# Kernel optimization log

Hardware: AMD Instinct MI355X
Metric: run time of the kernel (lower is better)

## Reference

```python
import jax, jax.numpy as jnp
import numpy as np

B, N, D, H = 4, 2048, 1024, 16
HD = D // H
LR_SCALE = 0.01  # base step size for the fast-weight test-time update
EPS = 1e-6


def setup_inputs() -> dict:
    key = jax.random.key(0)
    ks = jax.random.split(key, 11)
    s = 0.02
    x = jax.random.normal(ks[0], (B, N, D), jnp.float32)
    Wq = jax.random.normal(ks[1], (D, D), jnp.float32) * s
    Wk = jax.random.normal(ks[2], (D, D), jnp.float32) * s
    Wv = jax.random.normal(ks[3], (D, D), jnp.float32) * s
    Wo = jax.random.normal(ks[4], (D, D), jnp.float32) * s
    w1_init = jax.random.normal(ks[5], (H, HD, HD), jnp.float32) * s  # FastWeightGLU init state
    w3_init = jax.random.normal(ks[6], (H, HD, HD), jnp.float32) * s
    W_lr = jax.random.normal(ks[7], (D, H), jnp.float32) * s  # FastWeightHpGLU lr head
    norm_w = jnp.ones((D,), jnp.float32)  # grouped RMSNorm weight
    Wg1 = jax.random.normal(ks[8], (D, HD), jnp.float32) * s  # output_gate bottleneck
    Wg2 = jax.random.normal(ks[9], (HD, D), jnp.float32) * s
    return dict(x=x, Wq=Wq, Wk=Wk, Wv=Wv, Wo=Wo, w1_init=w1_init,
                w3_init=w3_init, W_lr=W_lr, norm_w=norm_w, Wg1=Wg1, Wg2=Wg2)


def _fast_weight_train(q, k, v, lr, w1_init, w3_init):
    # q,k,v: (b,n,h,hd); lr: (b,n,h); fast weight f(x) = silu(x@W1) * (x@W3)
    b = q.shape[0]
    W1_0 = jnp.broadcast_to(w1_init, (b,) + w1_init.shape)
    W3_0 = jnp.broadcast_to(w3_init, (b,) + w3_init.shape)

    def step(carry, inp):
        W1, W3 = carry
        q_t, k_t, v_t, lr_t = inp  # (b,h,hd), lr_t: (b,h,1)
        h1 = jnp.einsum('bhd,bhde->bhe', k_t, W1)
        h3 = jnp.einsum('bhd,bhde->bhe', k_t, W3)
        sg = jax.nn.sigmoid(h1)
        s1 = h1 * sg  # silu(h1)
        err = s1 * h3 - v_t  # d(0.5||f(k)-v||^2)/df
        dsilu = sg * (1.0 + h1 * (1.0 - sg))
        g1 = err * h3 * dsilu
        g3 = err * s1
        W1 = W1 - lr_t[..., None] * jnp.einsum('bhd,bhe->bhde', k_t, g1)
        W3 = W3 - lr_t[..., None] * jnp.einsum('bhd,bhe->bhde', k_t, g3)
        o1 = jnp.einsum('bhd,bhde->bhe', q_t, W1)
        o3 = jnp.einsum('bhd,bhde->bhe', q_t, W3)
        return (W1, W3), jax.nn.silu(o1) * o3

    xs = (q.transpose(1, 0, 2, 3), k.transpose(1, 0, 2, 3),
          v.transpose(1, 0, 2, 3), lr.transpose(1, 0, 2)[..., None])
    (W1, W3), outs = jax.lax.scan(step, (W1_0, W3_0), xs)
    return outs.transpose(1, 0, 2, 3), (W1, W3)  # (b,n,h,hd)


def reference(x, Wq, Wk, Wv, Wo, w1_init, w3_init, W_lr, norm_w, Wg1, Wg2):
    b, n, d = x.shape
    h = w1_init.shape[0]
    hd = d // h
    q = jax.nn.silu((x @ Wq).reshape(b, n, h, hd))
    k = jax.nn.silu((x @ Wk).reshape(b, n, h, hd))
    v = (x @ Wv).reshape(b, n, h, hd)
    lr = LR_SCALE * jax.nn.sigmoid(x @ W_lr)  # (b,n,h) per-token hyper-param
    out, _ = _fast_weight_train(q, k, v, lr, w1_init, w3_init)
    # grouped RMSNorm (per head) fused with sigmoid output gate
    rms = jax.lax.rsqrt(jnp.mean(out * out, axis=-1, keepdims=True) + EPS)
    out = (out * rms).reshape(b, n, d) * norm_w
    gate = (x @ Wg1) @ Wg2
    out = out * jax.nn.sigmoid(gate)
    return out @ Wo
```

## Files before the change

### kernel.cpp

```cpp
#include <hip/hip_runtime.h>
#include <hip/hip_bf16.h>

#define B_ 4
#define N_ 2048
#define D_ 1024
#define H_ 16
#define HD_ 64
#define MTOT (B_*N_)
#define CH_ 16
#define NCH_ (N_/CH_)

typedef __attribute__((ext_vector_type(8))) short short8v;
typedef __attribute__((ext_vector_type(4))) float f32x4;

__global__ void k_cast_bf16(const float* __restrict__ in, __hip_bfloat16* __restrict__ out, int n4){
  int i = blockIdx.x*256 + threadIdx.x;
  if (i >= n4) return;
  float4 vv = ((const float4*)in)[i];
  __hip_bfloat16 b0 = __float2bfloat16(vv.x), b1 = __float2bfloat16(vv.y),
                 b2 = __float2bfloat16(vv.z), b3 = __float2bfloat16(vv.w);
  ushort4 o;
  o.x = *(const unsigned short*)&b0; o.y = *(const unsigned short*)&b1;
  o.z = *(const unsigned short*)&b2; o.w = *(const unsigned short*)&b3;
  ((ushort4*)out)[i] = o;
}

__global__ void k_transpose_cast(const float* __restrict__ in, __hip_bfloat16* __restrict__ out,
                                 int R, int C){
  __shared__ float tile[64][65];
  int r0 = blockIdx.y*64, c0 = blockIdx.x*64;
  int tid = threadIdx.x;
  #pragma unroll
  for (int i=0;i<16;i++){ int idx = tid + i*256; int rr = idx>>6, cc = idx&63;
    tile[rr][cc] = in[(size_t)(r0+rr)*C + (c0+cc)]; }
  __syncthreads();
  #pragma unroll
  for (int i=0;i<16;i++){ int idx = tid + i*256; int rr = idx>>6, cc = idx&63;
    out[(size_t)(c0+rr)*R + (r0+cc)] = __float2bfloat16(tile[cc][rr]); }
}

__global__ void k_prep_wgl(const float* __restrict__ Wg1, const float* __restrict__ Wlr,
                           __hip_bfloat16* __restrict__ WgL){
  int idx = blockIdx.x*256 + threadIdx.x;
  int r = idx >> 10, d = idx & 1023;
  float v = 0.f;
  if (r < 64) v = Wg1[(size_t)d*64 + r];
  else if (r < 80) v = Wlr[(size_t)d*16 + (r-64)];
  WgL[idx] = __float2bfloat16(v);
}

__global__ void k_post_gl(const float* __restrict__ proj, __hip_bfloat16* __restrict__ t1,
                          float* __restrict__ lrout){
  int m = blockIdx.x*4 + (threadIdx.x>>6);
  int e = threadIdx.x & 63;
  float val = proj[(size_t)m*128 + e];
  t1[(size_t)m*64 + e] = __float2bfloat16(val);
  if (e < 16){
    float s = proj[(size_t)m*128 + 64 + e];
    lrout[(size_t)m*16 + e] = 0.01f/(1.0f+__expf(-s));
  }
}

__device__ __forceinline__ void gl2lds16(const void* g, void* l){
  __builtin_amdgcn_global_load_lds((const __attribute__((address_space(1))) void*)g,
                                   (__attribute__((address_space(3))) void*)l, 16, 0, 0);
}

template<int ACT, int LAYOUT>
__global__ __launch_bounds__(256,2) void k_gemm_bt2(
    const __hip_bfloat16* __restrict__ A, const __hip_bfloat16* __restrict__ BT,
    float* __restrict__ C, int M, int N, int K)
{
  __shared__ short As[128*32];
  __shared__ short Bs[128*32];
  const int n0 = blockIdx.x*128, m0 = blockIdx.y*128;
  const int tid = threadIdx.x, lane = tid & 63, wid = tid >> 6;
  const int wm = wid >> 1, wn = wid & 1;
  const short* Aps = (const short*)A;
  const short* Bps = (const short*)BT;
  f32x4 acc[4][4] = {};
  const int srow = wid*32 + (lane>>2);
  const int scol = (lane&3)*8;
  const size_t aoff0 = (size_t)(m0+srow)*K + scol;
  const size_t boff0 = (size_t)(n0+srow)*K + scol;
  short* lA = As + wid*1024;
  short* lB = Bs + wid*1024;
  const int row = lane & 15, kq = (lane >> 4)*8;
  for (int kk = 0; kk < K; kk += 32) {
    __syncthreads();
    gl2lds16(Aps + aoff0 + kk,                 lA);
    gl2lds16(Aps + aoff0 + (size_t)16*K + kk,  lA + 512);
    gl2lds16(Bps + boff0 + kk,                 lB);
    gl2lds16(Bps + boff0 + (size_t)16*K + kk,  lB + 512);
    __syncthreads();
    short8v af[4], bfr[4];
    #pragma unroll
    for (int i=0;i<4;i++) af[i]  = *(const short8v*)(As + (wm*64 + i*16 + row)*32 + kq);
    #pragma unroll
    for (int j=0;j<4;j++) bfr[j] = *(const short8v*)(Bs + (wn*64 + j*16 + row)*32 + kq);
    #pragma unroll
    for (int i=0;i<4;i++)
      #pragma unroll
      for (int j=0;j<4;j++)
        acc[i][j] = __builtin_amdgcn_mfma_f32_16x16x32_bf16(af[i], bfr[j], acc[i][j], 0, 0, 0);
  }
  #pragma unroll
  for (int i=0;i<4;i++){
    #pragma unroll
    for (int j=0;j<4;j++){
      int col = n0 + wn*64 + j*16 + (lane & 15);
      #pragma unroll
      for (int qq=0; qq<4; ++qq){
        int rowg = m0 + wm*64 + i*16 + (lane>>4)*4 + qq;
        float val = acc[i][j][qq];
        if (ACT==1) val = val/(1.0f+__expf(-val));
        if (LAYOUT==0) {
          C[(size_t)rowg*N + col] = val;
        } else {
          size_t oidx = ((((size_t)(rowg>>11))*16 + (col>>6))*(size_t)N_ + (size_t)(rowg & 2047))*64
                        + (size_t)(col & 63);
          C[oidx] = val;
        }
      }
    }
  }
}

__device__ __forceinline__ unsigned short bfr16(float x){
  __hip_bfloat16 b = __float2bfloat16(x);
  return *(unsigned short*)&b;
}
__device__ __forceinline__ short8v cvt_frag(const float4 a, const float4 c){
  short8v r;
  r[0]=(short)bfr16(a.x); r[1]=(short)bfr16(a.y); r[2]=(short)bfr16(a.z); r[3]=(short)bfr16(a.w);
  r[4]=(short)bfr16(c.x); r[5]=(short)bfr16(c.y); r[6]=(short)bfr16(c.z); r[7]=(short)bfr16(c.w);
  return r;
}

__global__ __launch_bounds__(256,1) void k_scan8(
    const float* __restrict__ q, const float* __restrict__ k, const float* __restrict__ v,
    const float* __restrict__ lr, const float* __restrict__ w1i, const float* __restrict__ w3i,
    float* __restrict__ so)
{
  const int blk = blockIdx.x;
  const int bh  = blk >> 2;
  const int sl  = blk & 3;
  const int b = bh >> 4, h = bh & 15;
  const int e0 = sl*16;
  const int tid = threadIdx.x, lane = tid & 63, wid = tid >> 6;
  const int tA = lane & 15, ks8 = (lane >> 4)*8;

  __shared__ __align__(16) __hip_bfloat16 Wb1[16*64];
  __shared__ __align__(16) __hip_bfloat16 Wb3[16*64];
  __shared__ __align__(16) float KW1e[256], KW3e[256];
  __shared__ __align__(16) float QW1[256], QW3[256];
  __shared__ __align__(16) float GKK[256], GQK[256];
  __shared__ __align__(16) float C13[512];

  const int we = tid & 15;
  const int wd = (tid >> 4) * 4;
  float w1r[4], w3r[4];
  {
    const float* w1p = w1i + (size_t)h*HD_*HD_ + e0 + we;
    const float* w3p = w3i + (size_t)h*HD_*HD_ + e0 + we;
    #pragma unroll
    for (int j=0;j<4;j++){ w1r[j] = w1p[(size_t)(wd+j)*64]; w3r[j] = w3p[(size_t)(wd+j)*64]; }
  }
  const int mir_off = we*128 + ((wd*2) ^ ((we&7)<<4));
  auto write_mirrors = [&](){
    uint2 p1, p3;
    p1.x = (unsigned)bfr16(w1r[0]) | ((unsigned)bfr16(w1r[1])<<16);
    p1.y = (unsigned)bfr16(w1r[2]) | ((unsigned)bfr16(w1r[3])<<16);
    p3.x = (unsigned)bfr16(w3r[0]) | ((unsigned)bfr16(w3r[1])<<16);
    p3.y = (unsigned)bfr16(w3r[2]) | ((unsigned)bfr16(w3r[3])<<16);
    *(uint2*)((char*)Wb1 + mir_off) = p1;
    *(uint2*)((char*)Wb3 + mir_off) = p3;
  };
  write_mirrors();

  const float* kfb = k + (size_t)bh*N_*64;
  const float* qfb = q + (size_t)bh*N_*64;
  const float* vfb = v + (size_t)bh*N_*64;
  const float* lrp = lr + ((size_t)b*N_)*16 + h;
  float* sob = so + (((size_t)b*N_)*16 + h)*64 + e0;

  auto mir_read = [&](const __hip_bfloat16* Wm, int m)->short8v{
    return *(const short8v*)((const char*)Wm + tA*128 + (((m*32+ks8)*2) ^ ((tA&7)<<4)));
  };

  float4 fA0,fA1,fA2,fA3;
  float4 fB0,fB1,fB2,fB3;
  float  vvr[16], lrr[16];

  if (wid >= 1) {
    const float* xr = ((wid==2) ? qfb : kfb) + (size_t)tA*64;
    fA0 = *(const float4*)(xr+ks8);    fA1 = *(const float4*)(xr+ks8+4);
    fA2 = *(const float4*)(xr+32+ks8); fA3 = *(const float4*)(xr+32+ks8+4);
    if (wid==3){
      const float* qr = qfb + (size_t)tA*64;
      fB0 = *(const float4*)(qr+ks8);    fB1 = *(const float4*)(qr+ks8+4);
      fB2 = *(const float4*)(qr+32+ks8); fB3 = *(const float4*)(qr+32+ks8+4);
    }
  } else if (lane < 16) {
    #pragma unroll
    for (int t=0;t<CH_;++t){
      vvr[t] = vfb[(size_t)t*64 + e0 + lane];
      lrr[t] = lrp[(size_t)t*16];
    }
  }
  __syncthreads();

  #pragma unroll 1
  for (int c = 0; c < NCH_; ++c) {
    const int t0 = c*CH_;

    if (wid == 1) {
      short8v af0 = cvt_frag(fA0,fA1), af1 = cvt_frag(fA2,fA3);
      const int slot = (((lane>>4)*4) ^ ((( tA>>1)&3)<<2));
      f32x4 acc = {};
      acc = __builtin_amdgcn_mfma_f32_16x16x32_bf16(af0, mir_read(Wb1,0), acc, 0,0,0);
      acc = __builtin_amdgcn_mfma_f32_16x16x32_bf16(af1, mir_read(Wb1,1), acc, 0,0,0);
      *(f32x4*)&KW1e[tA*16 + slot] = acc;
      f32x4 ac3 = {};
      ac3 = __builtin_amdgcn_mfma_f32_16x16x32_bf16(af0, mir_read(Wb3,0), ac3, 0,0,0);
      ac3 = __builtin_amdgcn_mfma_f32_16x16x32_bf16(af1, mir_read(Wb3,1), ac3, 0,0,0);
      *(f32x4*)&KW3e[tA*16 + slot] = ac3;
    } else if (wid == 2) {
      short8v af0 = cvt_frag(fA0,fA1), af1 = cvt_frag(fA2,fA3);
      f32x4 acc = {};
      acc = __builtin_amdgcn_mfma_f32_16x16x32_bf16(af0, mir_read(Wb1,0), acc, 0,0,0);
      acc = __builtin_amdgcn_mfma_f32_16x16x32_bf16(af1, mir_read(Wb1,1), acc, 0,0,0);
      #pragma unroll
      for (int qq=0;qq<4;++qq) QW1[((lane>>4)*4+qq)*16 + tA] = acc[qq];
      f32x4 ac3 = {};
      ac3 = __builtin_amdgcn_mfma_f32_16x16x32_bf16(af0, mir_read(Wb3,0), ac3, 0,0,0);
      ac3 = __builtin_amdgcn_mfma_f32_16x16x32_bf16(af1, mir_read(Wb3,1), ac3, 0,0,0);
      #pragma unroll
      for (int qq=0;qq<4;++qq) QW3[((lane>>4)*4+qq)*16 + tA] = ac3[qq];
    } else if (wid == 3) {
      short8v af0 = cvt_frag(fA0,fA1), af1 = cvt_frag(fA2,fA3);
      short8v aq0 = cvt_frag(fB0,fB1), aq1 = cvt_frag(fB2,fB3);
      f32x4 acc = {};
      acc = __builtin_amdgcn_mfma_f32_16x16x32_bf16(af0, af0, acc, 0,0,0);
      acc = __builtin_amdgcn_mfma_f32_16x16x32_bf16(af1, af1, acc, 0,0,0);
      #pragma unroll
      for (int qq=0;qq<4;++qq) GKK[((lane>>4)*4+qq)*16 + tA] = acc[qq];
      f32x4 ac2 = {};
      ac2 = __builtin_amdgcn_mfma_f32_16x16x32_bf16(aq0, af0, ac2, 0,0,0);
      ac2 = __builtin_amdgcn_mfma_f32_16x16x32_bf16(aq1, af1, ac2, 0,0,0);
      #pragma unroll
      for (int qq=0;qq<4;++qq) GQK[((lane>>4)*4+qq)*16 + tA] = ac2[qq];
    }
    __syncthreads();

    const int tn0 = ((c+1 < NCH_) ? c+1 : c) * CH_;
    if (wid >= 1) {
      const float* xr = ((wid==2) ? qfb : kfb) + (size_t)(tn0+tA)*64;
      fA0 = *(const float4*)(xr+ks8);    fA1 = *(const float4*)(xr+ks8+4);
      fA2 = *(const float4*)(xr+32+ks8); fA3 = *(const float4*)(xr+32+ks8+4);
      if (wid==3){
        const float* qr = qfb + (size_t)(tn0+tA)*64;
        fB0 = *(const float4*)(qr+ks8);    fB1 = *(const float4*)(qr+ks8+4);
        fB2 = *(const float4*)(qr+32+ks8); fB3 = *(const float4*)(qr+32+ks8+4);
      }
    } else if (lane < 16) {
      float vvn[16], lrn[16];
      #pragma unroll
      for (int t=0;t<CH_;++t){
        vvn[t] = vfb[(size_t)(tn0+t)*64 + e0 + lane];
        lrn[t] = lrp[(size_t)(tn0+t)*16];
      }
      float a1[16], a3[16];
      const int swr = ((lane>>1)&3)<<2;
      #pragma unroll
      for (int i2=0;i2<4;i2++){
        f32x4 x1 = *(const f32x4*)&KW1e[lane*16 + ((i2*4) ^ swr)];
        f32x4 x3 = *(const f32x4*)&KW3e[lane*16 + ((i2*4) ^ swr)];
        a1[i2*4+0]=x1[0]; a1[i2*4+1]=x1[1]; a1[i2*4+2]=x1[2]; a1[i2*4+3]=x1[3];
        a3[i2*4+0]=x3[0]; a3[i2*4+1]=x3[1]; a3[i2*4+2]=x3[2]; a3[i2*4+3]=x3[3];
      }
      f32x4 grow[3][4];
      #pragma unroll
      for (int i2=0;i2<4;i2++){
        grow[0][i2] = *(const f32x4*)&GKK[ 0 + i2*4];
        grow[1][i2] = *(const f32x4*)&GKK[16 + i2*4];
        grow[2][i2] = *(const f32x4*)&GKK[32 + i2*4];
      }
      #pragma unroll
      for (int t = 0; t < CH_; ++t) {
        const float h1 = a1[t], h3 = a3[t];
        const float sg = 1.0f/(1.0f + __expf(-h1));
        const float s1 = h1*sg;
        const float er = fmaf(s1, h3, -vvr[t]);
        const float ds = sg*fmaf(h1, 1.0f - sg, 1.0f);
        const float lt = lrr[t];
        float2 cc; cc.x = lt*(er*h3*ds); cc.y = lt*(er*s1);
        *(float2*)&C13[(t*16+lane)*2] = cc;
        #pragma unroll
        for (int t2 = t+1; t2 < CH_; ++t2) {
          const float g = grow[t%3][t2>>2][t2&3];
          a1[t2] = fmaf(-g, cc.x, a1[t2]);
          a3[t2] = fmaf(-g, cc.y, a3[t2]);
        }
        if (t + 3 < CH_) {
          #pragma unroll
          for (int i2=0;i2<4;i2++) grow[(t+3)%3][i2] = *(const f32x4*)&GKK[(t+3)*16 + i2*4];
        }
      }
      #pragma unroll
      for (int t=0;t<CH_;++t){ vvr[t]=vvn[t]; lrr[t]=lrn[t]; }
    }
    __syncthreads();

    {
      const int ot = tid >> 4, oe = tid & 15;
      float o1 = QW1[ot*16+oe], o3 = QW3[ot*16+oe];
      #pragma unroll
      for (int s = 0; s < CH_; ++s) {
        const float gl2 = GQK[ot*16+s];
        const float2 cc = *(const float2*)&C13[(s*16+oe)*2];
        const float g = (s <= ot) ? gl2 : 0.0f;
        o1 = fmaf(-g, cc.x, o1);
        o3 = fmaf(-g, cc.y, o3);
      }
      sob[(size_t)(t0+ot)*(H_*HD_) + oe] = (o1/(1.0f + __expf(-o1)))*o3;
    }

    #pragma unroll
    for (int s = 0; s < CH_; ++s) {
      const float2 cc = *(const float2*)&C13[(s*16+we)*2];
      const float4 ks = *(const float4*)(kfb + (size_t)(t0+s)*64 + wd);
      w1r[0] = fmaf(-ks.x, cc.x, w1r[0]); w1r[1] = fmaf(-ks.y, cc.x, w1r[1]);
      w1r[2] = fmaf(-ks.z, cc.x, w1r[2]); w1r[3] = fmaf(-ks.w, cc.x, w1r[3]);
      w3r[0] = fmaf(-ks.x, cc.y, w3r[0]); w3r[1] = fmaf(-ks.y, cc.y, w3r[1]);
      w3r[2] = fmaf(-ks.z, cc.y, w3r[2]); w3r[3] = fmaf(-ks.w, cc.y, w3r[3]);
    }
    write_mirrors();
    __syncthreads();
  }
}

__global__ void k_norm_gate(const float* __restrict__ so, const float* __restrict__ gate,
                            const float* __restrict__ nw, __hip_bfloat16* __restrict__ y)
{
  int idx = blockIdx.x*4 + (threadIdx.x>>6);
  int e = threadIdx.x & 63;
  float o = so[(size_t)idx*64 + e];
  float ss = o*o;
  #pragma unroll
  for (int m=32; m>=1; m>>=1) ss += __shfl_xor(ss, m, 64);
  float rms = rsqrtf(ss*(1.0f/64.0f) + 1e-6f);
  int hh = idx & 15;
  size_t bn = (size_t)(idx >> 4);
  int d = hh*64 + e;
  float g = gate[bn*1024 + d];
  float val = o*rms*nw[d] * (1.0f/(1.0f+__expf(-g)));
  y[bn*1024 + d] = __float2bfloat16(val);
}

extern "C" void kernel_launch(void* const* d_in, const int* in_sizes, int n_in,
                              void* d_out, int out_size, void* d_ws, size_t ws_size,
                              hipStream_t stream)
{
  const float* x   = (const float*)d_in[0];
  const float* Wq  = (const float*)d_in[1];
  const float* Wk  = (const float*)d_in[2];
  const float* Wv  = (const float*)d_in[3];
  const float* Wo  = (const float*)d_in[4];
  const float* w1i = (const float*)d_in[5];
  const float* w3i = (const float*)d_in[6];
  const float* Wlr = (const float*)d_in[7];
  const float* nw  = (const float*)d_in[8];
  const float* Wg1 = (const float*)d_in[9];
  const float* Wg2 = (const float*)d_in[10];
  float* out = (float*)d_out;

  char* p = (char*)d_ws;
  auto take = [&](size_t bytes)->void*{ void* r = (void*)p; p += (bytes + 255) & ~(size_t)255; return r; };
  __hip_bfloat16* xb   = (__hip_bfloat16*)take((size_t)MTOT*D_*2);
  __hip_bfloat16* Wqt  = (__hip_bfloat16*)take((size_t)D_*D_*2);
  __hip_bfloat16* Wkt  = (__hip_bfloat16*)take((size_t)D_*D_*2);
  __hip_bfloat16* Wvt  = (__hip_bfloat16*)take((size_t)D_*D_*2);
  __hip_bfloat16* Wot  = (__hip_bfloat16*)take((size_t)D_*D_*2);
  __hip_bfloat16* Wg2t = (__hip_bfloat16*)take((size_t)D_*HD_*2);
  __hip_bfloat16* WgL  = (__hip_bfloat16*)take((size_t)128*D_*2);
  __hip_bfloat16* t1b  = (__hip_bfloat16*)take((size_t)MTOT*HD_*2);
  float* projt = (float*)take((size_t)MTOT*128*4);
  float* qf  = (float*)take((size_t)MTOT*D_*4);
  float* kf  = (float*)take((size_t)MTOT*D_*4);
  float* vf  = (float*)take((size_t)MTOT*D_*4);
  float* lrb = (float*)take((size_t)MTOT*H_*4);
  float* sob = (float*)take((size_t)MTOT*D_*4);
  __hip_bfloat16* yb = (__hip_bfloat16*)take((size_t)MTOT*D_*2);

  k_cast_bf16<<<MTOT*D_/4/256, 256, 0, stream>>>(x, xb, MTOT*D_/4);
  k_transpose_cast<<<dim3(16,16), 256, 0, stream>>>(Wq, Wqt, D_, D_);
  k_transpose_cast<<<dim3(16,16), 256, 0, stream>>>(Wk, Wkt, D_, D_);
  k_transpose_cast<<<dim3(16,16), 256, 0, stream>>>(Wv, Wvt, D_, D_);
  k_transpose_cast<<<dim3(16,16), 256, 0, stream>>>(Wo, Wot, D_, D_);
  k_transpose_cast<<<dim3(16,1),  256, 0, stream>>>(Wg2, Wg2t, HD_, D_);
  k_prep_wgl<<<512, 256, 0, stream>>>(Wg1, Wlr, WgL);
  k_gemm_bt2<0,0><<<dim3(1,64), 256, 0, stream>>>(xb, WgL, projt, MTOT, 128, D_);
  k_post_gl<<<MTOT/4, 256, 0, stream>>>(projt, t1b, lrb);
  k_gemm_bt2<1,1><<<dim3(8,64), 256, 0, stream>>>(xb, Wqt, qf, MTOT, D_, D_);
  k_gemm_bt2<1,1><<<dim3(8,64), 256, 0, stream>>>(xb, Wkt, kf, MTOT, D_, D_);
  k_gemm_bt2<0,1><<<dim3(8,64), 256, 0, stream>>>(xb, Wvt, vf, MTOT, D_, D_);
  k_gemm_bt2<0,0><<<dim3(8,64), 256, 0, stream>>>(t1b, Wg2t, out, MTOT, D_, HD_);
  k_scan8<<<256, 256, 0, stream>>>(qf, kf, vf, lrb, w1i, w3i, sob);
  k_norm_gate<<<MTOT*H_/4, 256, 0, stream>>>(sob, out, nw, yb);
  k_gemm_bt2<0,0><<<dim3(8,64), 256, 0, stream>>>(yb, Wot, out, MTOT, D_, D_);
}
```

Baseline: 607.6 us.

## Pipeline next-chunk projections in scan with double-buffered LDS and rank-16 correction

```diff
diff --git a/kernel.cpp b/kernel.cpp
--- a/kernel.cpp
+++ b/kernel.cpp
@@ -137,7 +137,7 @@
   return r;
 }
 
-__global__ __launch_bounds__(256,1) void k_scan8(
+__global__ __launch_bounds__(256,1) void k_scan10(
     const float* __restrict__ q, const float* __restrict__ k, const float* __restrict__ v,
     const float* __restrict__ lr, const float* __restrict__ w1i, const float* __restrict__ w3i,
     float* __restrict__ so)
@@ -152,9 +152,10 @@
 
   __shared__ __align__(16) __hip_bfloat16 Wb1[16*64];
   __shared__ __align__(16) __hip_bfloat16 Wb3[16*64];
-  __shared__ __align__(16) float KW1e[256], KW3e[256];
-  __shared__ __align__(16) float QW1[256], QW3[256];
-  __shared__ __align__(16) float GKK[256], GQK[256];
+  __shared__ __align__(16) float KW1e[2][256], KW3e[2][256];
+  __shared__ __align__(16) float QW1[2][256],  QW3[2][256];
+  __shared__ __align__(16) float GKK[2][256],  GQK[2][256];
+  __shared__ __align__(16) float G2KK[256], G2QK[256];
   __shared__ __align__(16) float C13[512];
 
   const int we = tid & 15;
@@ -190,6 +191,7 @@
 
   float4 fA0,fA1,fA2,fA3;
   float4 fB0,fB1,fB2,fB3;
+  short8v kp0, kp1;
   float  vvr[16], lrr[16];
 
   if (wid >= 1) {
@@ -210,60 +212,122 @@
   }
   __syncthreads();
 
+  if (wid == 1) {
+    short8v xa0 = cvt_frag(fA0,fA1), xa1 = cvt_frag(fA2,fA3);
+    const int slot = (((lane>>4)*4) ^ (((tA>>1)&3)<<2));
+    f32x4 acc = {};
+    acc = __builtin_amdgcn_mfma_f32_16x16x32_bf16(xa0, mir_read(Wb1,0), acc, 0,0,0);
+    acc = __builtin_amdgcn_mfma_f32_16x16x32_bf16(xa1, mir_read(Wb1,1), acc, 0,0,0);
+    *(f32x4*)&KW1e[0][tA*16 + slot] = acc;
+    f32x4 ac3 = {};
+    ac3 = __builtin_amdgcn_mfma_f32_16x16x32_bf16(xa0, mir_read(Wb3,0), ac3, 0,0,0);
+    ac3 = __builtin_amdgcn_mfma_f32_16x16x32_bf16(xa1, mir_read(Wb3,1), ac3, 0,0,0);
+    *(f32x4*)&KW3e[0][tA*16 + slot] = ac3;
+  } else if (wid == 2) {
+    short8v xa0 = cvt_frag(fA0,fA1), xa1 = cvt_frag(fA2,fA3);
+    f32x4 acc = {};
+    acc = __builtin_amdgcn_mfma_f32_16x16x32_bf16(xa0, mir_read(Wb1,0), acc, 0,0,0);
+    acc = __builtin_amdgcn_mfma_f32_16x16x32_bf16(xa1, mir_read(Wb1,1), acc, 0,0,0);
+    #pragma unroll
+    for (int qq=0;qq<4;++qq) QW1[0][((lane>>4)*4+qq)*16 + tA] = acc[qq];
+    f32x4 ac3 = {};
+    ac3 = __builtin_amdgcn_mfma_f32_16x16x32_bf16(xa0, mir_read(Wb3,0), ac3, 0,0,0);
+    ac3 = __builtin_amdgcn_mfma_f32_16x16x32_bf16(xa1, mir_read(Wb3,1), ac3, 0,0,0);
+    #pragma unroll
+    for (int qq=0;qq<4;++qq) QW3[0][((lane>>4)*4+qq)*16 + tA] = ac3[qq];
+  } else if (wid == 3) {
+    short8v xa0 = cvt_frag(fA0,fA1), xa1 = cvt_frag(fA2,fA3);
+    short8v qa0 = cvt_frag(fB0,fB1), qa1 = cvt_frag(fB2,fB3);
+    f32x4 acc = {};
+    acc = __builtin_amdgcn_mfma_f32_16x16x32_bf16(xa0, xa0, acc, 0,0,0);
+    acc = __builtin_amdgcn_mfma_f32_16x16x32_bf16(xa1, xa1, acc, 0,0,0);
+    #pragma unroll
+    for (int qq=0;qq<4;++qq) GKK[0][((lane>>4)*4+qq)*16 + tA] = acc[qq];
+    f32x4 ac2 = {};
+    ac2 = __builtin_amdgcn_mfma_f32_16x16x32_bf16(qa0, xa0, ac2, 0,0,0);
+    ac2 = __builtin_amdgcn_mfma_f32_16x16x32_bf16(qa1, xa1, ac2, 0,0,0);
+    #pragma unroll
+    for (int qq=0;qq<4;++qq) GQK[0][((lane>>4)*4+qq)*16 + tA] = ac2[qq];
+    kp0 = xa0; kp1 = xa1;
+  }
+  if (wid >= 1) {
+    const float* xr = ((wid==2) ? qfb : kfb) + (size_t)(CH_+tA)*64;
+    fA0 = *(const float4*)(xr+ks8);    fA1 = *(const float4*)(xr+ks8+4);
+    fA2 = *(const float4*)(xr+32+ks8); fA3 = *(const float4*)(xr+32+ks8+4);
+    if (wid==3){
+      const float* qr = qfb + (size_t)(CH_+tA)*64;
+      fB0 = *(const float4*)(qr+ks8);    fB1 = *(const float4*)(qr+ks8+4);
+      fB2 = *(const float4*)(qr+32+ks8); fB3 = *(const float4*)(qr+32+ks8+4);
+    }
+  }
+  __syncthreads();
+
   #pragma unroll 1
   for (int c = 0; c < NCH_; ++c) {
     const int t0 = c*CH_;
-
-    if (wid == 1) {
-      short8v af0 = cvt_frag(fA0,fA1), af1 = cvt_frag(fA2,fA3);
-      const int slot = (((lane>>4)*4) ^ ((( tA>>1)&3)<<2));
-      f32x4 acc = {};
-      acc = __builtin_amdgcn_mfma_f32_16x16x32_bf16(af0, mir_read(Wb1,0), acc, 0,0,0);
-      acc = __builtin_amdgcn_mfma_f32_16x16x32_bf16(af1, mir_read(Wb1,1), acc, 0,0,0);
-      *(f32x4*)&KW1e[tA*16 + slot] = acc;
-      f32x4 ac3 = {};
-      ac3 = __builtin_amdgcn_mfma_f32_16x16x32_bf16(af0, mir_read(Wb3,0), ac3, 0,0,0);
-      ac3 = __builtin_amdgcn_mfma_f32_16x16x32_bf16(af1, mir_read(Wb3,1), ac3, 0,0,0);
-      *(f32x4*)&KW3e[tA*16 + slot] = ac3;
-    } else if (wid == 2) {
-      short8v af0 = cvt_frag(fA0,fA1), af1 = cvt_frag(fA2,fA3);
-      f32x4 acc = {};
-      acc = __builtin_amdgcn_mfma_f32_16x16x32_bf16(af0, mir_read(Wb1,0), acc, 0,0,0);
-      acc = __builtin_amdgcn_mfma_f32_16x16x32_bf16(af1, mir_read(Wb1,1), acc, 0,0,0);
-      #pragma unroll
-      for (int qq=0;qq<4;++qq) QW1[((lane>>4)*4+qq)*16 + tA] = acc[qq];
-      f32x4 ac3 = {};
-      ac3 = __builtin_amdgcn_mfma_f32_16x16x32_bf16(af0, mir_read(Wb3,0), ac3, 0,0,0);
-      ac3 = __builtin_amdgcn_mfma_f32_16x16x32_bf16(af1, mir_read(Wb3,1), ac3, 0,0,0);
-      #pragma unroll
-      for (int qq=0;qq<4;++qq) QW3[((lane>>4)*4+qq)*16 + tA] = ac3[qq];
-    } else if (wid == 3) {
-      short8v af0 = cvt_frag(fA0,fA1), af1 = cvt_frag(fA2,fA3);
-      short8v aq0 = cvt_frag(fB0,fB1), aq1 = cvt_frag(fB2,fB3);
-      f32x4 acc = {};
-      acc = __builtin_amdgcn_mfma_f32_16x16x32_bf16(af0, af0, acc, 0,0,0);
-      acc = __builtin_amdgcn_mfma_f32_16x16x32_bf16(af1, af1, acc, 0,0,0);
-      #pragma unroll
-      for (int qq=0;qq<4;++qq) GKK[((lane>>4)*4+qq)*16 + tA] = acc[qq];
-      f32x4 ac2 = {};
-      ac2 = __builtin_amdgcn_mfma_f32_16x16x32_bf16(aq0, af0, ac2, 0,0,0);
-      ac2 = __builtin_amdgcn_mfma_f32_16x16x32_bf16(aq1, af1, ac2, 0,0,0);
-      #pragma unroll
-      for (int qq=0;qq<4;++qq) GQK[((lane>>4)*4+qq)*16 + tA] = ac2[qq];
-    }
-    __syncthreads();
-
-    const int tn0 = ((c+1 < NCH_) ? c+1 : c) * CH_;
+    const int p  = c & 1;
+    const int pn = p ^ 1;
+
     if (wid >= 1) {
-      const float* xr = ((wid==2) ? qfb : kfb) + (size_t)(tn0+tA)*64;
-      fA0 = *(const float4*)(xr+ks8);    fA1 = *(const float4*)(xr+ks8+4);
-      fA2 = *(const float4*)(xr+32+ks8); fA3 = *(const float4*)(xr+32+ks8+4);
-      if (wid==3){
-        const float* qr = qfb + (size_t)(tn0+tA)*64;
-        fB0 = *(const float4*)(qr+ks8);    fB1 = *(const float4*)(qr+ks8+4);
-        fB2 = *(const float4*)(qr+32+ks8); fB3 = *(const float4*)(qr+32+ks8+4);
+      if (c+1 < NCH_) {
+        short8v xa0 = cvt_frag(fA0,fA1), xa1 = cvt_frag(fA2,fA3);
+        if (wid == 1) {
+          const int slot = (((lane>>4)*4) ^ (((tA>>1)&3)<<2));
+          f32x4 acc = {};
+          acc = __builtin_amdgcn_mfma_f32_16x16x32_bf16(xa0, mir_read(Wb1,0), acc, 0,0,0);
+          acc = __builtin_amdgcn_mfma_f32_16x16x32_bf16(xa1, mir_read(Wb1,1), acc, 0,0,0);
+          *(f32x4*)&KW1e[pn][tA*16 + slot] = acc;
+          f32x4 ac3 = {};
+          ac3 = __builtin_amdgcn_mfma_f32_16x16x32_bf16(xa0, mir_read(Wb3,0), ac3, 0,0,0);
+          ac3 = __builtin_amdgcn_mfma_f32_16x16x32_bf16(xa1, mir_read(Wb3,1), ac3, 0,0,0);
+          *(f32x4*)&KW3e[pn][tA*16 + slot] = ac3;
+        } else if (wid == 2) {
+          f32x4 acc = {};
+          acc = __builtin_amdgcn_mfma_f32_16x16x32_bf16(xa0, mir_read(Wb1,0), acc, 0,0,0);
+          acc = __builtin_amdgcn_mfma_f32_16x16x32_bf16(xa1, mir_read(Wb1,1), acc, 0,0,0);
+          #pragma unroll
+          for (int qq=0;qq<4;++qq) QW1[pn][((lane>>4)*4+qq)*16 + tA] = acc[qq];
+          f32x4 ac3 = {};
+          ac3 = __builtin_amdgcn_mfma_f32_16x16x32_bf16(xa0, mir_read(Wb3,0), ac3, 0,0,0);
+          ac3 = __builtin_amdgcn_mfma_f32_16x16x32_bf16(xa1, mir_read(Wb3,1), ac3, 0,0,0);
+          #pragma unroll
+          for (int qq=0;qq<4;++qq) QW3[pn][((lane>>4)*4+qq)*16 + tA] = ac3[qq];
+        } else {
+          short8v qa0 = cvt_frag(fB0,fB1), qa1 = cvt_frag(fB2,fB3);
+          f32x4 acc = {};
+          acc = __builtin_amdgcn_mfma_f32_16x16x32_bf16(xa0, xa0, acc, 0,0,0);
+          acc = __builtin_amdgcn_mfma_f32_16x16x32_bf16(xa1, xa1, acc, 0,0,0);
+          #pragma unroll
+          for (int qq=0;qq<4;++qq) GKK[pn][((lane>>4)*4+qq)*16 + tA] = acc[qq];
+          f32x4 ac2 = {};
+          ac2 = __builtin_amdgcn_mfma_f32_16x16x32_bf16(qa0, xa0, ac2, 0,0,0);
+          ac2 = __builtin_amdgcn_mfma_f32_16x16x32_bf16(qa1, xa1, ac2, 0,0,0);
+          #pragma unroll
+          for (int qq=0;qq<4;++qq) GQK[pn][((lane>>4)*4+qq)*16 + tA] = ac2[qq];
+          f32x4 a2k = {};
+          a2k = __builtin_amdgcn_mfma_f32_16x16x32_bf16(xa0, kp0, a2k, 0,0,0);
+          a2k = __builtin_amdgcn_mfma_f32_16x16x32_bf16(xa1, kp1, a2k, 0,0,0);
+          #pragma unroll
+          for (int qq=0;qq<4;++qq) G2KK[((lane>>4)*4+qq)*16 + tA] = a2k[qq];
+          f32x4 a2q = {};
+          a2q = __builtin_amdgcn_mfma_f32_16x16x32_bf16(qa0, kp0, a2q, 0,0,0);
+          a2q = __builtin_amdgcn_mfma_f32_16x16x32_bf16(qa1, kp1, a2q, 0,0,0);
+          #pragma unroll
+          for (int qq=0;qq<4;++qq) G2QK[((lane>>4)*4+qq)*16 + tA] = a2q[qq];
+          kp0 = xa0; kp1 = xa1;
+        }
+        const int tn0 = ((c+2 < NCH_) ? c+2 : NCH_-1) * CH_;
+        const float* xr = ((wid==2) ? qfb : kfb) + (size_t)(tn0+tA)*64;
+        fA0 = *(const float4*)(xr+ks8);    fA1 = *(const float4*)(xr+ks8+4);
+        fA2 = *(const float4*)(xr+32+ks8); fA3 = *(const float4*)(xr+32+ks8+4);
+        if (wid==3){
+          const float* qr = qfb + (size_t)(tn0+tA)*64;
+          fB0 = *(const float4*)(qr+ks8);    fB1 = *(const float4*)(qr+ks8+4);
+          fB2 = *(const float4*)(qr+32+ks8); fB3 = *(const float4*)(qr+32+ks8+4);
+        }
       }
     } else if (lane < 16) {
+      const int tn0 = ((c+1 < NCH_) ? c+1 : c) * CH_;
       float vvn[16], lrn[16];
       #pragma unroll
       for (int t=0;t<CH_;++t){
@@ -274,17 +338,17 @@
       const int swr = ((lane>>1)&3)<<2;
       #pragma unroll
       for (int i2=0;i2<4;i2++){
-        f32x4 x1 = *(const f32x4*)&KW1e[lane*16 + ((i2*4) ^ swr)];
-        f32x4 x3 = *(const f32x4*)&KW3e[lane*16 + ((i2*4) ^ swr)];
+        f32x4 x1 = *(const f32x4*)&KW1e[p][lane*16 + ((i2*4) ^ swr)];
+        f32x4 x3 = *(const f32x4*)&KW3e[p][lane*16 + ((i2*4) ^ swr)];
         a1[i2*4+0]=x1[0]; a1[i2*4+1]=x1[1]; a1[i2*4+2]=x1[2]; a1[i2*4+3]=x1[3];
         a3[i2*4+0]=x3[0]; a3[i2*4+1]=x3[1]; a3[i2*4+2]=x3[2]; a3[i2*4+3]=x3[3];
       }
       f32x4 grow[3][4];
       #pragma unroll
       for (int i2=0;i2<4;i2++){
-        grow[0][i2] = *(const f32x4*)&GKK[ 0 + i2*4];
-        grow[1][i2] = *(const f32x4*)&GKK[16 + i2*4];
-        grow[2][i2] = *(const f32x4*)&GKK[32 + i2*4];
+        grow[0][i2] = *(const f32x4*)&GKK[p][ 0 + i2*4];
+        grow[1][i2] = *(const f32x4*)&GKK[p][16 + i2*4];
+        grow[2][i2] = *(const f32x4*)&GKK[p][32 + i2*4];
       }
       #pragma unroll
       for (int t = 0; t < CH_; ++t) {
@@ -304,7 +368,7 @@
         }
         if (t + 3 < CH_) {
           #pragma unroll
-          for (int i2=0;i2<4;i2++) grow[(t+3)%3][i2] = *(const f32x4*)&GKK[(t+3)*16 + i2*4];
+          for (int i2=0;i2<4;i2++) grow[(t+3)%3][i2] = *(const f32x4*)&GKK[p][(t+3)*16 + i2*4];
         }
       }
       #pragma unroll
@@ -314,28 +378,54 @@
 
     {
       const int ot = tid >> 4, oe = tid & 15;
-      float o1 = QW1[ot*16+oe], o3 = QW3[ot*16+oe];
+      const bool doc = (c+1 < NCH_);
+      float gq[16], g2k[16], g2q[16];
+      #pragma unroll
+      for (int i2=0;i2<4;i2++){
+        f32x4 a = *(const f32x4*)&GQK[p][ot*16 + i2*4];
+        gq[i2*4]=a[0]; gq[i2*4+1]=a[1]; gq[i2*4+2]=a[2]; gq[i2*4+3]=a[3];
+      }
+      if (doc){
+        #pragma unroll
+        for (int i2=0;i2<4;i2++){
+          f32x4 a = *(const f32x4*)&G2KK[ot*16 + i2*4];
+          f32x4 bq = *(const f32x4*)&G2QK[ot*16 + i2*4];
+          g2k[i2*4]=a[0]; g2k[i2*4+1]=a[1]; g2k[i2*4+2]=a[2]; g2k[i2*4+3]=a[3];
+          g2q[i2*4]=bq[0]; g2q[i2*4+1]=bq[1]; g2q[i2*4+2]=bq[2]; g2q[i2*4+3]=bq[3];
+        }
+      }
+      float o1 = QW1[p][ot*16+oe], o3 = QW3[p][ot*16+oe];
+      float ao1=0.f, ao3=0.f, ak1=0.f, ak3=0.f, aq1=0.f, aq3=0.f;
       #pragma unroll
       for (int s = 0; s < CH_; ++s) {
-        const float gl2 = GQK[ot*16+s];
         const float2 cc = *(const float2*)&C13[(s*16+oe)*2];
-        const float g = (s <= ot) ? gl2 : 0.0f;
-        o1 = fmaf(-g, cc.x, o1);
-        o3 = fmaf(-g, cc.y, o3);
-      }
+        const float go = (s <= ot) ? gq[s] : 0.0f;
+        ao1 = fmaf(go, cc.x, ao1);  ao3 = fmaf(go, cc.y, ao3);
+        if (doc){
+          ak1 = fmaf(g2k[s], cc.x, ak1);  ak3 = fmaf(g2k[s], cc.y, ak3);
+          aq1 = fmaf(g2q[s], cc.x, aq1);  aq3 = fmaf(g2q[s], cc.y, aq3);
+        }
+      }
+      o1 -= ao1; o3 -= ao3;
       sob[(size_t)(t0+ot)*(H_*HD_) + oe] = (o1/(1.0f + __expf(-o1)))*o3;
+      if (doc){
+        const int ie = oe*16 + ((((ot>>2)<<2) ^ (((oe>>1)&3)<<2))) + (ot&3);
+        KW1e[pn][ie] -= ak1;
+        KW3e[pn][ie] -= ak3;
+        QW1[pn][ot*16+oe] -= aq1;
+        QW3[pn][ot*16+oe] -= aq3;
+      }
+      #pragma unroll
+      for (int s = 0; s < CH_; ++s) {
+        const float2 cc = *(const float2*)&C13[(s*16+we)*2];
+        const float4 ks = *(const float4*)(kfb + (size_t)(t0+s)*64 + wd);
+        w1r[0] = fmaf(-ks.x, cc.x, w1r[0]); w1r[1] = fmaf(-ks.y, cc.x, w1r[1]);
+        w1r[2] = fmaf(-ks.z, cc.x, w1r[2]); w1r[3] = fmaf(-ks.w, cc.x, w1r[3]);
+        w3r[0] = fmaf(-ks.x, cc.y, w3r[0]); w3r[1] = fmaf(-ks.y, cc.y, w3r[1]);
+        w3r[2] = fmaf(-ks.z, cc.y, w3r[2]); w3r[3] = fmaf(-ks.w, cc.y, w3r[3]);
+      }
+      write_mirrors();
     }
-
-    #pragma unroll
-    for (int s = 0; s < CH_; ++s) {
-      const float2 cc = *(const float2*)&C13[(s*16+we)*2];
-      const float4 ks = *(const float4*)(kfb + (size_t)(t0+s)*64 + wd);
-      w1r[0] = fmaf(-ks.x, cc.x, w1r[0]); w1r[1] = fmaf(-ks.y, cc.x, w1r[1]);
-      w1r[2] = fmaf(-ks.z, cc.x, w1r[2]); w1r[3] = fmaf(-ks.w, cc.x, w1r[3]);
-      w3r[0] = fmaf(-ks.x, cc.y, w3r[0]); w3r[1] = fmaf(-ks.y, cc.y, w3r[1]);
-      w3r[2] = fmaf(-ks.z, cc.y, w3r[2]); w3r[3] = fmaf(-ks.w, cc.y, w3r[3]);
-    }
-    write_mirrors();
     __syncthreads();
   }
 }
@@ -406,7 +496,7 @@
   k_gemm_bt2<1,1><<<dim3(8,64), 256, 0, stream>>>(xb, Wkt, kf, MTOT, D_, D_);
   k_gemm_bt2<0,1><<<dim3(8,64), 256, 0, stream>>>(xb, Wvt, vf, MTOT, D_, D_);
   k_gemm_bt2<0,0><<<dim3(8,64), 256, 0, stream>>>(t1b, Wg2t, out, MTOT, D_, HD_);
-  k_scan8<<<256, 256, 0, stream>>>(qf, kf, vf, lrb, w1i, w3i, sob);
+  k_scan10<<<256, 256, 0, stream>>>(qf, kf, vf, lrb, w1i, w3i, sob);
   k_norm_gate<<<MTOT*H_/4, 256, 0, stream>>>(sob, out, nw, yb);
   k_gemm_bt2<0,0><<<dim3(8,64), 256, 0, stream>>>(yb, Wot, out, MTOT, D_, D_);
 }
```

Result: slower. 626.5 us (+3.1%).

## Collapse fast-weight scan block to a single wavefront with register-resident weights

Applied to the files above, without the earlier changes.

```diff
diff --git a/kernel.cpp b/kernel.cpp
--- a/kernel.cpp
+++ b/kernel.cpp
@@ -137,7 +137,7 @@
   return r;
 }
 
-__global__ __launch_bounds__(256,1) void k_scan8(
+__global__ __launch_bounds__(64,1) void k_scan11(
     const float* __restrict__ q, const float* __restrict__ k, const float* __restrict__ v,
     const float* __restrict__ lr, const float* __restrict__ w1i, const float* __restrict__ w3i,
     float* __restrict__ so)
@@ -147,36 +147,15 @@
   const int sl  = blk & 3;
   const int b = bh >> 4, h = bh & 15;
   const int e0 = sl*16;
-  const int tid = threadIdx.x, lane = tid & 63, wid = tid >> 6;
-  const int tA = lane & 15, ks8 = (lane >> 4)*8;
-
-  __shared__ __align__(16) __hip_bfloat16 Wb1[16*64];
-  __shared__ __align__(16) __hip_bfloat16 Wb3[16*64];
+  const int lane = threadIdx.x;
+  const int tA = lane & 15, g = lane >> 4;
+
   __shared__ __align__(16) float KW1e[256], KW3e[256];
   __shared__ __align__(16) float QW1[256], QW3[256];
   __shared__ __align__(16) float GKK[256], GQK[256];
   __shared__ __align__(16) float C13[512];
-
-  const int we = tid & 15;
-  const int wd = (tid >> 4) * 4;
-  float w1r[4], w3r[4];
-  {
-    const float* w1p = w1i + (size_t)h*HD_*HD_ + e0 + we;
-    const float* w3p = w3i + (size_t)h*HD_*HD_ + e0 + we;
-    #pragma unroll
-    for (int j=0;j<4;j++){ w1r[j] = w1p[(size_t)(wd+j)*64]; w3r[j] = w3p[(size_t)(wd+j)*64]; }
-  }
-  const int mir_off = we*128 + ((wd*2) ^ ((we&7)<<4));
-  auto write_mirrors = [&](){
-    uint2 p1, p3;
-    p1.x = (unsigned)bfr16(w1r[0]) | ((unsigned)bfr16(w1r[1])<<16);
-    p1.y = (unsigned)bfr16(w1r[2]) | ((unsigned)bfr16(w1r[3])<<16);
-    p3.x = (unsigned)bfr16(w3r[0]) | ((unsigned)bfr16(w3r[1])<<16);
-    p3.y = (unsigned)bfr16(w3r[2]) | ((unsigned)bfr16(w3r[3])<<16);
-    *(uint2*)((char*)Wb1 + mir_off) = p1;
-    *(uint2*)((char*)Wb3 + mir_off) = p3;
-  };
-  write_mirrors();
+  __shared__ __align__(16) float vS[256];
+  __shared__ float lrS[16];
 
   const float* kfb = k + (size_t)bh*N_*64;
   const float* qfb = q + (size_t)bh*N_*64;
@@ -184,92 +163,94 @@
   const float* lrp = lr + ((size_t)b*N_)*16 + h;
   float* sob = so + (((size_t)b*N_)*16 + h)*64 + e0;
 
-  auto mir_read = [&](const __hip_bfloat16* Wm, int m)->short8v{
-    return *(const short8v*)((const char*)Wm + tA*128 + (((m*32+ks8)*2) ^ ((tA&7)<<4)));
-  };
-
-  float4 fA0,fA1,fA2,fA3;
-  float4 fB0,fB1,fB2,fB3;
-  float  vvr[16], lrr[16];
-
-  if (wid >= 1) {
-    const float* xr = ((wid==2) ? qfb : kfb) + (size_t)tA*64;
-    fA0 = *(const float4*)(xr+ks8);    fA1 = *(const float4*)(xr+ks8+4);
-    fA2 = *(const float4*)(xr+32+ks8); fA3 = *(const float4*)(xr+32+ks8+4);
-    if (wid==3){
-      const float* qr = qfb + (size_t)tA*64;
-      fB0 = *(const float4*)(qr+ks8);    fB1 = *(const float4*)(qr+ks8+4);
-      fB2 = *(const float4*)(qr+32+ks8); fB3 = *(const float4*)(qr+32+ks8+4);
-    }
-  } else if (lane < 16) {
-    #pragma unroll
-    for (int t=0;t<CH_;++t){
-      vvr[t] = vfb[(size_t)t*64 + e0 + lane];
-      lrr[t] = lrp[(size_t)t*16];
-    }
-  }
-  __syncthreads();
+  float w1m[2][8], w3m[2][8];
+  {
+    const float* w1p = w1i + (size_t)h*HD_*HD_ + e0 + tA;
+    const float* w3p = w3i + (size_t)h*HD_*HD_ + e0 + tA;
+    #pragma unroll
+    for (int m=0;m<2;m++)
+      #pragma unroll
+      for (int j=0;j<8;j++){
+        const int d = m*32 + g*8 + j;
+        w1m[m][j] = w1p[(size_t)d*64];
+        w3m[m][j] = w3p[(size_t)d*64];
+      }
+  }
+  short8v wb1[2], wb3[2];
+  #pragma unroll
+  for (int m=0;m<2;m++){
+    short8v r1, r3;
+    #pragma unroll
+    for (int j=0;j<8;j++){ r1[j]=(short)bfr16(w1m[m][j]); r3[j]=(short)bfr16(w3m[m][j]); }
+    wb1[m]=r1; wb3[m]=r3;
+  }
+
+  float4 kP[4], qP[4]; float vP[4]; float lrP = 0.f;
+  {
+    const float* kr = kfb + (size_t)tA*64 + g*8;
+    const float* qr = qfb + (size_t)tA*64 + g*8;
+    #pragma unroll
+    for (int m=0;m<2;m++){
+      kP[m*2]   = *(const float4*)(kr + m*32);
+      kP[m*2+1] = *(const float4*)(kr + m*32 + 4);
+      qP[m*2]   = *(const float4*)(qr + m*32);
+      qP[m*2+1] = *(const float4*)(qr + m*32 + 4);
+    }
+    #pragma unroll
+    for (int i=0;i<4;i++) vP[i] = vfb[(size_t)(g*4+i)*64 + e0 + tA];
+    if (lane < 16) lrP = lrp[(size_t)lane*16];
+  }
 
   #pragma unroll 1
   for (int c = 0; c < NCH_; ++c) {
     const int t0 = c*CH_;
-
-    if (wid == 1) {
-      short8v af0 = cvt_frag(fA0,fA1), af1 = cvt_frag(fA2,fA3);
-      const int slot = (((lane>>4)*4) ^ ((( tA>>1)&3)<<2));
-      f32x4 acc = {};
-      acc = __builtin_amdgcn_mfma_f32_16x16x32_bf16(af0, mir_read(Wb1,0), acc, 0,0,0);
-      acc = __builtin_amdgcn_mfma_f32_16x16x32_bf16(af1, mir_read(Wb1,1), acc, 0,0,0);
-      *(f32x4*)&KW1e[tA*16 + slot] = acc;
-      f32x4 ac3 = {};
-      ac3 = __builtin_amdgcn_mfma_f32_16x16x32_bf16(af0, mir_read(Wb3,0), ac3, 0,0,0);
-      ac3 = __builtin_amdgcn_mfma_f32_16x16x32_bf16(af1, mir_read(Wb3,1), ac3, 0,0,0);
-      *(f32x4*)&KW3e[tA*16 + slot] = ac3;
-    } else if (wid == 2) {
-      short8v af0 = cvt_frag(fA0,fA1), af1 = cvt_frag(fA2,fA3);
-      f32x4 acc = {};
-      acc = __builtin_amdgcn_mfma_f32_16x16x32_bf16(af0, mir_read(Wb1,0), acc, 0,0,0);
-      acc = __builtin_amdgcn_mfma_f32_16x16x32_bf16(af1, mir_read(Wb1,1), acc, 0,0,0);
-      #pragma unroll
-      for (int qq=0;qq<4;++qq) QW1[((lane>>4)*4+qq)*16 + tA] = acc[qq];
-      f32x4 ac3 = {};
-      ac3 = __builtin_amdgcn_mfma_f32_16x16x32_bf16(af0, mir_read(Wb3,0), ac3, 0,0,0);
-      ac3 = __builtin_amdgcn_mfma_f32_16x16x32_bf16(af1, mir_read(Wb3,1), ac3, 0,0,0);
-      #pragma unroll
-      for (int qq=0;qq<4;++qq) QW3[((lane>>4)*4+qq)*16 + tA] = ac3[qq];
-    } else if (wid == 3) {
-      short8v af0 = cvt_frag(fA0,fA1), af1 = cvt_frag(fA2,fA3);
-      short8v aq0 = cvt_frag(fB0,fB1), aq1 = cvt_frag(fB2,fB3);
-      f32x4 acc = {};
-      acc = __builtin_amdgcn_mfma_f32_16x16x32_bf16(af0, af0, acc, 0,0,0);
-      acc = __builtin_amdgcn_mfma_f32_16x16x32_bf16(af1, af1, acc, 0,0,0);
-      #pragma unroll
-      for (int qq=0;qq<4;++qq) GKK[((lane>>4)*4+qq)*16 + tA] = acc[qq];
-      f32x4 ac2 = {};
-      ac2 = __builtin_amdgcn_mfma_f32_16x16x32_bf16(aq0, af0, ac2, 0,0,0);
-      ac2 = __builtin_amdgcn_mfma_f32_16x16x32_bf16(aq1, af1, ac2, 0,0,0);
-      #pragma unroll
-      for (int qq=0;qq<4;++qq) GQK[((lane>>4)*4+qq)*16 + tA] = ac2[qq];
-    }
-    __syncthreads();
-
-    const int tn0 = ((c+1 < NCH_) ? c+1 : c) * CH_;
-    if (wid >= 1) {
-      const float* xr = ((wid==2) ? qfb : kfb) + (size_t)(tn0+tA)*64;
-      fA0 = *(const float4*)(xr+ks8);    fA1 = *(const float4*)(xr+ks8+4);
-      fA2 = *(const float4*)(xr+32+ks8); fA3 = *(const float4*)(xr+32+ks8+4);
-      if (wid==3){
-        const float* qr = qfb + (size_t)(tn0+tA)*64;
-        fB0 = *(const float4*)(qr+ks8);    fB1 = *(const float4*)(qr+ks8+4);
-        fB2 = *(const float4*)(qr+32+ks8); fB3 = *(const float4*)(qr+32+ks8+4);
-      }
-    } else if (lane < 16) {
-      float vvn[16], lrn[16];
-      #pragma unroll
-      for (int t=0;t<CH_;++t){
-        vvn[t] = vfb[(size_t)(tn0+t)*64 + e0 + lane];
-        lrn[t] = lrp[(size_t)(tn0+t)*16];
-      }
+    #pragma unroll
+    for (int i=0;i<4;i++) vS[(g*4+i)*16 + tA] = vP[i];
+    if (lane < 16) lrS[lane] = lrP;
+    short8v ka0 = cvt_frag(kP[0],kP[1]), ka1 = cvt_frag(kP[2],kP[3]);
+    short8v qa0 = cvt_frag(qP[0],qP[1]), qa1 = cvt_frag(qP[2],qP[3]);
+    const int tn0 = ((c+1 < NCH_) ? (c+1) : c)*CH_;
+    {
+      const float* kr = kfb + (size_t)(tn0+tA)*64 + g*8;
+      const float* qr = qfb + (size_t)(tn0+tA)*64 + g*8;
+      #pragma unroll
+      for (int m=0;m<2;m++){
+        kP[m*2]   = *(const float4*)(kr + m*32);
+        kP[m*2+1] = *(const float4*)(kr + m*32 + 4);
+        qP[m*2]   = *(const float4*)(qr + m*32);
+        qP[m*2+1] = *(const float4*)(qr + m*32 + 4);
+      }
+      #pragma unroll
+      for (int i=0;i<4;i++) vP[i] = vfb[(size_t)(tn0+g*4+i)*64 + e0 + tA];
+      if (lane < 16) lrP = lrp[(size_t)(tn0+lane)*16];
+    }
+    f32x4 aKW1={}, aKW3={}, aQW1={}, aQW3={}, aGKK={}, aGQK={};
+    aKW1 = __builtin_amdgcn_mfma_f32_16x16x32_bf16(ka0, wb1[0], aKW1, 0,0,0);
+    aKW1 = __builtin_amdgcn_mfma_f32_16x16x32_bf16(ka1, wb1[1], aKW1, 0,0,0);
+    aKW3 = __builtin_amdgcn_mfma_f32_16x16x32_bf16(ka0, wb3[0], aKW3, 0,0,0);
+    aKW3 = __builtin_amdgcn_mfma_f32_16x16x32_bf16(ka1, wb3[1], aKW3, 0,0,0);
+    aQW1 = __builtin_amdgcn_mfma_f32_16x16x32_bf16(qa0, wb1[0], aQW1, 0,0,0);
+    aQW1 = __builtin_amdgcn_mfma_f32_16x16x32_bf16(qa1, wb1[1], aQW1, 0,0,0);
+    aQW3 = __builtin_amdgcn_mfma_f32_16x16x32_bf16(qa0, wb3[0], aQW3, 0,0,0);
+    aQW3 = __builtin_amdgcn_mfma_f32_16x16x32_bf16(qa1, wb3[1], aQW3, 0,0,0);
+    aGKK = __builtin_amdgcn_mfma_f32_16x16x32_bf16(ka0, ka0, aGKK, 0,0,0);
+    aGKK = __builtin_amdgcn_mfma_f32_16x16x32_bf16(ka1, ka1, aGKK, 0,0,0);
+    aGQK = __builtin_amdgcn_mfma_f32_16x16x32_bf16(qa0, ka0, aGQK, 0,0,0);
+    aGQK = __builtin_amdgcn_mfma_f32_16x16x32_bf16(qa1, ka1, aGQK, 0,0,0);
+    const int slot = (g*4) ^ (((tA>>1)&3)<<2);
+    *(f32x4*)&KW1e[tA*16 + slot] = aKW1;
+    *(f32x4*)&KW3e[tA*16 + slot] = aKW3;
+    #pragma unroll
+    for (int qq=0;qq<4;++qq){
+      QW1[(g*4+qq)*16 + tA] = aQW1[qq];
+      QW3[(g*4+qq)*16 + tA] = aQW3[qq];
+      GKK[(g*4+qq)*16 + tA] = aGKK[qq];
+      GQK[(g*4+qq)*16 + tA] = aGQK[qq];
+    }
+    asm volatile("s_waitcnt lgkmcnt(0)" ::: "memory");
+    __builtin_amdgcn_sched_barrier(0);
+
+    if (lane < 16) {
       float a1[16], a3[16];
       const int swr = ((lane>>1)&3)<<2;
       #pragma unroll
@@ -291,52 +272,78 @@
         const float h1 = a1[t], h3 = a3[t];
         const float sg = 1.0f/(1.0f + __expf(-h1));
         const float s1 = h1*sg;
-        const float er = fmaf(s1, h3, -vvr[t]);
+        const float er = fmaf(s1, h3, -vS[t*16+lane]);
         const float ds = sg*fmaf(h1, 1.0f - sg, 1.0f);
-        const float lt = lrr[t];
+        const float lt = lrS[t];
         float2 cc; cc.x = lt*(er*h3*ds); cc.y = lt*(er*s1);
         *(float2*)&C13[(t*16+lane)*2] = cc;
         #pragma unroll
         for (int t2 = t+1; t2 < CH_; ++t2) {
-          const float g = grow[t%3][t2>>2][t2&3];
-          a1[t2] = fmaf(-g, cc.x, a1[t2]);
-          a3[t2] = fmaf(-g, cc.y, a3[t2]);
+          const float gg = grow[t%3][t2>>2][t2&3];
+          a1[t2] = fmaf(-gg, cc.x, a1[t2]);
+          a3[t2] = fmaf(-gg, cc.y, a3[t2]);
         }
         if (t + 3 < CH_) {
           #pragma unroll
           for (int i2=0;i2<4;i2++) grow[(t+3)%3][i2] = *(const f32x4*)&GKK[(t+3)*16 + i2*4];
         }
       }
-      #pragma unroll
-      for (int t=0;t<CH_;++t){ vvr[t]=vvn[t]; lrr[t]=lrn[t]; }
-    }
-    __syncthreads();
-
-    {
-      const int ot = tid >> 4, oe = tid & 15;
-      float o1 = QW1[ot*16+oe], o3 = QW3[ot*16+oe];
-      #pragma unroll
-      for (int s = 0; s < CH_; ++s) {
-        const float gl2 = GQK[ot*16+s];
-        const float2 cc = *(const float2*)&C13[(s*16+oe)*2];
-        const float g = (s <= ot) ? gl2 : 0.0f;
-        o1 = fmaf(-g, cc.x, o1);
-        o3 = fmaf(-g, cc.y, o3);
-      }
-      sob[(size_t)(t0+ot)*(H_*HD_) + oe] = (o1/(1.0f + __expf(-o1)))*o3;
-    }
-
-    #pragma unroll
-    for (int s = 0; s < CH_; ++s) {
-      const float2 cc = *(const float2*)&C13[(s*16+we)*2];
-      const float4 ks = *(const float4*)(kfb + (size_t)(t0+s)*64 + wd);
-      w1r[0] = fmaf(-ks.x, cc.x, w1r[0]); w1r[1] = fmaf(-ks.y, cc.x, w1r[1]);
-      w1r[2] = fmaf(-ks.z, cc.x, w1r[2]); w1r[3] = fmaf(-ks.w, cc.x, w1r[3]);
-      w3r[0] = fmaf(-ks.x, cc.y, w3r[0]); w3r[1] = fmaf(-ks.y, cc.y, w3r[1]);
-      w3r[2] = fmaf(-ks.z, cc.y, w3r[2]); w3r[3] = fmaf(-ks.w, cc.y, w3r[3]);
-    }
-    write_mirrors();
-    __syncthreads();
+    }
+    asm volatile("s_waitcnt lgkmcnt(0)" ::: "memory");
+    __builtin_amdgcn_sched_barrier(0);
+
+    float c1r[16], c3r[16];
+    #pragma unroll
+    for (int s=0;s<CH_;++s){
+      float2 cc = *(const float2*)&C13[(s*16+tA)*2];
+      c1r[s]=cc.x; c3r[s]=cc.y;
+    }
+    #pragma unroll
+    for (int i=0;i<4;++i){
+      const int ot = g*4 + i;
+      float o1 = QW1[ot*16+tA], o3 = QW3[ot*16+tA];
+      float gq[16];
+      #pragma unroll
+      for (int i2=0;i2<4;i2++){
+        f32x4 a = *(const f32x4*)&GQK[ot*16 + i2*4];
+        gq[i2*4]=a[0]; gq[i2*4+1]=a[1]; gq[i2*4+2]=a[2]; gq[i2*4+3]=a[3];
+      }
+      #pragma unroll
+      for (int s=0;s<CH_;++s){
+        const float gg = (s <= ot) ? gq[s] : 0.0f;
+        o1 = fmaf(-gg, c1r[s], o1);
+        o3 = fmaf(-gg, c3r[s], o3);
+      }
+      sob[(size_t)(t0+ot)*(H_*HD_) + tA] = (o1/(1.0f + __expf(-o1)))*o3;
+    }
+
+    #pragma unroll
+    for (int s=0;s<CH_;++s){
+      const float* kr = kfb + (size_t)(t0+s)*64 + g*8;
+      const float4 k0 = *(const float4*)(kr);
+      const float4 k1 = *(const float4*)(kr+4);
+      const float4 k2 = *(const float4*)(kr+32);
+      const float4 k3 = *(const float4*)(kr+36);
+      const float c1 = c1r[s], c3 = c3r[s];
+      float kk0[8] = {k0.x,k0.y,k0.z,k0.w,k1.x,k1.y,k1.z,k1.w};
+      float kk1[8] = {k2.x,k2.y,k2.z,k2.w,k3.x,k3.y,k3.z,k3.w};
+      #pragma unroll
+      for (int j=0;j<8;j++){
+        w1m[0][j] = fmaf(-kk0[j], c1, w1m[0][j]);
+        w3m[0][j] = fmaf(-kk0[j], c3, w3m[0][j]);
+        w1m[1][j] = fmaf(-kk1[j], c1, w1m[1][j]);
+        w3m[1][j] = fmaf(-kk1[j], c3, w3m[1][j]);
+      }
+    }
+    #pragma unroll
+    for (int m=0;m<2;m++){
+      short8v r1, r3;
+      #pragma unroll
+      for (int j=0;j<8;j++){ r1[j]=(short)bfr16(w1m[m][j]); r3[j]=(short)bfr16(w3m[m][j]); }
+      wb1[m]=r1; wb3[m]=r3;
+    }
+    asm volatile("s_waitcnt lgkmcnt(0)" ::: "memory");
+    __builtin_amdgcn_sched_barrier(0);
   }
 }
 
@@ -406,7 +413,7 @@
   k_gemm_bt2<1,1><<<dim3(8,64), 256, 0, stream>>>(xb, Wkt, kf, MTOT, D_, D_);
   k_gemm_bt2<0,1><<<dim3(8,64), 256, 0, stream>>>(xb, Wvt, vf, MTOT, D_, D_);
   k_gemm_bt2<0,0><<<dim3(8,64), 256, 0, stream>>>(t1b, Wg2t, out, MTOT, D_, HD_);
-  k_scan8<<<256, 256, 0, stream>>>(qf, kf, vf, lrb, w1i, w3i, sob);
+  k_scan11<<<256, 64, 0, stream>>>(qf, kf, vf, lrb, w1i, w3i, sob);
   k_norm_gate<<<MTOT*H_/4, 256, 0, stream>>>(sob, out, nw, yb);
   k_gemm_bt2<0,0><<<dim3(8,64), 256, 0, stream>>>(yb, Wot, out, MTOT, D_, D_);
 }
```

Result: slower. 802.1 us (+32.0%).
